# Performance work log

Measured on AMD Instinct MI355X. Metric: run time of the kernel, lower is better.

Reference implementation:

```python
import jax, jax.numpy as jnp
import numpy as np

D_MODEL = 1024
NUM_HEAD = 16
D_K = D_MODEL // NUM_HEAD


def setup_inputs() -> dict:
    key = jax.random.key(0)
    ks = jax.random.split(key, 9)
    s = 1.0 / np.sqrt(D_MODEL)
    x = jax.random.normal(ks[0], (2, 2048, D_MODEL), dtype=jnp.float32)
    Wq = jax.random.uniform(ks[1], (D_MODEL, D_MODEL), jnp.float32, -s, s)
    bq = jax.random.uniform(ks[2], (D_MODEL,), jnp.float32, -s, s)
    Wk = jax.random.uniform(ks[3], (D_MODEL, D_MODEL), jnp.float32, -s, s)
    bk = jax.random.uniform(ks[4], (D_MODEL,), jnp.float32, -s, s)
    Wv = jax.random.uniform(ks[5], (D_MODEL, D_MODEL), jnp.float32, -s, s)
    bv = jax.random.uniform(ks[6], (D_MODEL,), jnp.float32, -s, s)
    Wo = jax.random.uniform(ks[7], (D_MODEL, D_MODEL), jnp.float32, -s, s)
    bo = jax.random.uniform(ks[8], (D_MODEL,), jnp.float32, -s, s)
    return {"x": x, "Wq": Wq, "bq": bq, "Wk": Wk, "bk": bk,
            "Wv": Wv, "bv": bv, "Wo": Wo, "bo": bo}


def reference(x, Wq, bq, Wk, bk, Wv, bv, Wo, bo):
    b, n, d = x.shape
    h, dk = NUM_HEAD, D_K
    # Linear projections (torch Linear: x @ W.T + b)
    q = (x @ Wq.T + bq).reshape(b, n, h, dk).transpose(0, 2, 1, 3)  # [b,h,n,dk]
    k = (x @ Wk.T + bk).reshape(b, n, h, dk).transpose(0, 2, 1, 3)
    v = (x @ Wv.T + bv).reshape(b, n, h, dk).transpose(0, 2, 1, 3)
    scores = jnp.einsum('bhqd,bhkd->bhqk', q, k) / jnp.sqrt(jnp.float32(dk))
    attn = jax.nn.softmax(scores, axis=-1)  # [b,h,n,n]
    out = jnp.einsum('bhqk,bhkd->bhqd', attn, v)
    out = out.transpose(0, 2, 1, 3).reshape(b, n, d)
    return out @ Wo.T + bo
```

## Files before the change

### kernel.cpp

```cpp
#include <hip/hip_runtime.h>

#define BATCH   2
#define SEQ     2048
#define DMODEL  1024
#define NHEAD   16
#define DKH     64
#define MTOT    (BATCH*SEQ)
#define KDIM    DMODEL

#define XB    0u
#define WQB   (4u*1024u*1024u)
#define WKB   (5u*1024u*1024u)
#define WVB   (6u*1024u*1024u)
#define WOB   (7u*1024u*1024u)
#define QOFF  (8u*1024u*1024u)
#define KOFF  (12u*1024u*1024u)
#define VOFF  (16u*1024u*1024u)
#define OOFF  (20u*1024u*1024u)

typedef __bf16 bf16x8 __attribute__((ext_vector_type(8)));
typedef __bf16 bf16x4 __attribute__((ext_vector_type(4)));
typedef float  f32x4  __attribute__((ext_vector_type(4)));
typedef float  f32x16 __attribute__((ext_vector_type(16)));

__device__ __forceinline__ void async16(const __bf16* g, __bf16* l) {
  __builtin_amdgcn_global_load_lds(
      (const __attribute__((address_space(1))) void*)g,
      (__attribute__((address_space(3))) void*)l, 16, 0, 0);
}

__device__ __forceinline__ unsigned cvtpk_bf16(float lo, float hi) {
  unsigned r;
  asm("v_cvt_pk_bf16_f32 %0, %1, %2" : "=v"(r) : "v"(lo), "v"(hi));
  return r;
}
__device__ __forceinline__ void plswap(unsigned& a, unsigned& b) {
  asm("v_permlane32_swap_b32 %0, %1" : "+v"(a), "+v"(b));
}

__global__ __launch_bounds__(256) void cvt_fp32_bf16(
    const float* __restrict__ x,  const float* __restrict__ wq,
    const float* __restrict__ wk, const float* __restrict__ wv,
    const float* __restrict__ wo, __bf16* __restrict__ ws)
{
  const float* src; __bf16* dst; int n;
  switch (blockIdx.y) {
    case 0:  src = x;  dst = ws + XB;  n = 4 * 1024 * 1024; break;
    case 1:  src = wq; dst = ws + WQB; n = 1024 * 1024;     break;
    case 2:  src = wk; dst = ws + WKB; n = 1024 * 1024;     break;
    case 3:  src = wv; dst = ws + WVB; n = 1024 * 1024;     break;
    default: src = wo; dst = ws + WOB; n = 1024 * 1024;     break;
  }
  const int i = (blockIdx.x * 256 + threadIdx.x) * 8;
  if (i < n) {
    const float4 a = *(const float4*)(src + i);
    const float4 b = *(const float4*)(src + i + 4);
    bf16x8 o;
    o[0] = (__bf16)a.x; o[1] = (__bf16)a.y; o[2] = (__bf16)a.z; o[3] = (__bf16)a.w;
    o[4] = (__bf16)b.x; o[5] = (__bf16)b.y; o[6] = (__bf16)b.z; o[7] = (__bf16)b.w;
    *(bf16x8*)(dst + i) = o;
  }
}

__device__ __forceinline__ void gemm128_core(
    const __bf16* __restrict__ A, const __bf16* __restrict__ W,
    int m0, int n0, __bf16* lds, f32x4 (&acc)[4][4])
{
  __bf16* A_lds = lds;
  __bf16* B_lds = lds + 4096;
  const int t    = threadIdx.x;
  const int w    = t >> 6;
  const int lane = t & 63;
  const int ln15 = lane & 15;
  const int quad = lane >> 4;
  const int wr   = (w >> 1) << 6;
  const int wc   = (w & 1) << 6;

#pragma unroll
  for (int i = 0; i < 4; ++i)
#pragma unroll
    for (int j = 0; j < 4; ++j) acc[i][j] = (f32x4){0.f, 0.f, 0.f, 0.f};

  for (int kt = 0; kt < KDIM; kt += 32) {
    __syncthreads();
#pragma unroll
    for (int issue = 0; issue < 2; ++issue) {
      const int cbase = issue * 256 + (w << 6);
      const int c     = cbase + lane;
      const int row   = c >> 2;
      const int goff  = ((c & 3) ^ (row & 3)) << 3;
      async16(A + (size_t)(m0 + row) * KDIM + kt + goff, A_lds + cbase * 8);
      async16(W + (size_t)(n0 + row) * KDIM + kt + goff, B_lds + cbase * 8);
    }
    __syncthreads();

    bf16x8 af[4], bfr[4];
#pragma unroll
    for (int i = 0; i < 4; ++i) {
      const int row = wr + i * 16 + ln15;
      af[i] = *(const bf16x8*)&A_lds[row * 32 + ((quad ^ (row & 3)) << 3)];
    }
#pragma unroll
    for (int j = 0; j < 4; ++j) {
      const int row = wc + j * 16 + ln15;
      bfr[j] = *(const bf16x8*)&B_lds[row * 32 + ((quad ^ (row & 3)) << 3)];
    }
#pragma unroll
    for (int i = 0; i < 4; ++i)
#pragma unroll
      for (int j = 0; j < 4; ++j)
        acc[i][j] = __builtin_amdgcn_mfma_f32_16x16x32_bf16(af[i], bfr[j], acc[i][j], 0, 0, 0);
  }
}

__global__ __launch_bounds__(256) void qkv_gemm(
    const __bf16* __restrict__ X,
    const __bf16* __restrict__ Wq, const float* __restrict__ bq,
    const __bf16* __restrict__ Wk, const float* __restrict__ bk,
    const __bf16* __restrict__ Wv, const float* __restrict__ bv,
    __bf16* __restrict__ ws)
{
  __shared__ __align__(16) __bf16 lds[128 * 64];

  const int z = blockIdx.z;
  const __bf16* W    = (z == 0) ? Wq : (z == 1) ? Wk : Wv;
  const float*  bias = (z == 0) ? bq : (z == 1) ? bk : bv;
  __bf16* out = ws + ((z == 0) ? QOFF : (z == 1) ? KOFF : VOFF);
  const float scale = (z == 0) ? 0.125f * 1.44269504088896f : 1.0f;

  const int m0 = blockIdx.x * 128;
  const int n0 = blockIdx.y * 128;

  f32x4 acc[4][4];
  gemm128_core(X, W, m0, n0, lds, acc);

  const int t = threadIdx.x, w = t >> 6, lane = t & 63;
  const int ln15 = lane & 15, quad = lane >> 4;
  const int wr = (w >> 1) << 6, wc = (w & 1) << 6;

  float bj4[4];
#pragma unroll
  for (int j = 0; j < 4; ++j) bj4[j] = bias[n0 + wc + j * 16 + ln15];

  __syncthreads();
  __bf16* scr = lds + (w << 10);

  const int bb = m0 >> 11;
  const int s_base = (m0 & 2047) + wr;
  const int h = (n0 + wc) >> 6;

  if (z != 2) {
    const int rdrow = lane & 15, rdseg = lane >> 4;
#pragma unroll
    for (int i = 0; i < 4; ++i) {
#pragma unroll
      for (int j = 0; j < 4; ++j)
#pragma unroll
        for (int rr = 0; rr < 4; ++rr)
          scr[(quad * 4 + rr) * 64 + j * 16 + ln15] =
              (__bf16)((acc[i][j][rr] + bj4[j]) * scale);
      bf16x8 v0 = *(const bf16x8*)&scr[rdrow * 64 + rdseg * 16];
      bf16x8 v1 = *(const bf16x8*)&scr[rdrow * 64 + rdseg * 16 + 8];
      const int s = s_base + i * 16 + rdrow;
      __bf16* p = out + (((size_t)(bb * NHEAD + h)) * SEQ + s) * DKH + rdseg * 16;
      *(bf16x8*)p = v0;
      *(bf16x8*)&p[8] = v1;
    }
  } else {
#pragma unroll
    for (int i = 0; i < 4; ++i) {
#pragma unroll
      for (int j = 0; j < 4; ++j) {
        bf16x4 pk;
#pragma unroll
        for (int rr = 0; rr < 4; ++rr) pk[rr] = (__bf16)(acc[i][j][rr] + bj4[j]);
        *(bf16x4*)&scr[(j * 16 + ln15) * 16 + quad * 4] = pk;
      }
      bf16x8 c0 = *(const bf16x8*)&scr[lane * 16];
      bf16x8 c1 = *(const bf16x8*)&scr[lane * 16 + 8];
      __bf16* p = out + (((size_t)(bb * NHEAD + h)) * DKH + lane) * SEQ
                      + s_base + i * 16;
      *(bf16x8*)p = c0;
      *(bf16x8*)&p[8] = c1;
    }
  }
}

__global__ __launch_bounds__(256) void out_gemm(
    const __bf16* __restrict__ A, const __bf16* __restrict__ Wo,
    const float* __restrict__ bo, float* __restrict__ out)
{
  __shared__ __align__(16) __bf16 lds[6144];
  __bf16* A_lds = lds;
  __bf16* B_lds = lds + 2048;

  const int m0 = blockIdx.x * 64;
  const int n0 = blockIdx.y * 128;

  const int t = threadIdx.x, w = t >> 6, lane = t & 63;
  const int ln15 = lane & 15, quad = lane >> 4;

  f32x4 acc[4][2];
#pragma unroll
  for (int i = 0; i < 4; ++i)
#pragma unroll
    for (int j = 0; j < 2; ++j) acc[i][j] = (f32x4){0.f, 0.f, 0.f, 0.f};

  for (int kt = 0; kt < KDIM; kt += 32) {
    __syncthreads();
    {
      const int c = (w << 6) + lane;
      const int row = c >> 2;
      const int goff = ((c & 3) ^ (row & 3)) << 3;
      async16(A + (size_t)(m0 + row) * KDIM + kt + goff, A_lds + c * 8);
    }
#pragma unroll
    for (int issue = 0; issue < 2; ++issue) {
      const int cbase = issue * 256 + (w << 6);
      const int c = cbase + lane;
      const int row = c >> 2;
      const int goff = ((c & 3) ^ (row & 3)) << 3;
      async16(Wo + (size_t)(n0 + row) * KDIM + kt + goff, B_lds + cbase * 8);
    }
    __syncthreads();

    bf16x8 af[4], bfr[2];
#pragma unroll
    for (int i = 0; i < 4; ++i) {
      const int row = i * 16 + ln15;
      af[i] = *(const bf16x8*)&A_lds[row * 32 + ((quad ^ (row & 3)) << 3)];
    }
#pragma unroll
    for (int j = 0; j < 2; ++j) {
      const int row = (w << 5) + j * 16 + ln15;
      bfr[j] = *(const bf16x8*)&B_lds[row * 32 + ((quad ^ (row & 3)) << 3)];
    }
#pragma unroll
    for (int i = 0; i < 4; ++i)
#pragma unroll
      for (int j = 0; j < 2; ++j)
        acc[i][j] = __builtin_amdgcn_mfma_f32_16x16x32_bf16(af[i], bfr[j], acc[i][j], 0, 0, 0);
  }

  float bj2[2];
#pragma unroll
  for (int j = 0; j < 2; ++j) bj2[j] = bo[n0 + (w << 5) + j * 16 + ln15];

  __syncthreads();
  float* scrf = (float*)lds + (w << 9);

  const int rdrow = lane & 15, rdseg = lane >> 4;
#pragma unroll
  for (int i = 0; i < 4; ++i) {
#pragma unroll
    for (int j = 0; j < 2; ++j) {
      f32x4 v;
#pragma unroll
      for (int rr = 0; rr < 4; ++rr) v[rr] = acc[i][j][rr] + bj2[j];
      *(f32x4*)&scrf[(j * 16 + ln15) * 16 + quad * 4] = v;
    }
    const int m = m0 + i * 16 + rdrow;
    float* p = out + (size_t)m * DMODEL + n0 + (w << 5) + rdseg * 8;
#pragma unroll
    for (int cc = 0; cc < 2; ++cc) {
      f32x4 v;
#pragma unroll
      for (int e = 0; e < 4; ++e)
        v[e] = scrf[(rdseg * 8 + cc * 4 + e) * 16 + rdrow];
      *(f32x4*)&p[cc * 4] = v;
    }
  }
}

__device__ __forceinline__ void softmax_frag(const f32x16& s, float& l,
                                             bf16x8& pfa, bf16x8& pfb)
{
  float p[16];
#pragma unroll
  for (int r = 0; r < 16; ++r) {
    p[r] = __builtin_amdgcn_exp2f(s[r]);
    l += p[r];
  }
  unsigned A0 = cvtpk_bf16(p[0],  p[1]);
  unsigned A1 = cvtpk_bf16(p[2],  p[3]);
  unsigned B0 = cvtpk_bf16(p[4],  p[5]);
  unsigned B1 = cvtpk_bf16(p[6],  p[7]);
  unsigned C0 = cvtpk_bf16(p[8],  p[9]);
  unsigned C1 = cvtpk_bf16(p[10], p[11]);
  unsigned D0 = cvtpk_bf16(p[12], p[13]);
  unsigned D1 = cvtpk_bf16(p[14], p[15]);
  plswap(A0, B0);
  plswap(A1, B1);
  plswap(C0, D0);
  plswap(C1, D1);
  union { unsigned u[4]; bf16x8 v; } ua, ub;
  ua.u[0] = A0; ua.u[1] = A1; ua.u[2] = B0; ua.u[3] = B1;
  ub.u[0] = C0; ub.u[1] = C1; ub.u[2] = D0; ub.u[3] = D1;
  pfa = ua.v;
  pfb = ub.v;
}

__global__ __launch_bounds__(512, 4) void attn_kernel(
    const __bf16* __restrict__ Qb, const __bf16* __restrict__ Kb,
    const __bf16* __restrict__ Vtb, __bf16* __restrict__ Ob)
{
  __shared__ __align__(16) __bf16 smem[3 * 128 * 64];
  __bf16* QP = smem;
  __bf16* Ks = smem + 8192;
  __bf16* Vs = smem + 16384;

  const int t = threadIdx.x, w = t >> 6, lane = t & 63;
  const int ln31 = lane & 31, hl = lane >> 5;
  const int g  = w & 3;
  const int kh = w >> 2;
  const int bh = blockIdx.x;
  const int q0 = blockIdx.y * 128;
  const int bb = bh >> 4, hh = bh & 15;

  const __bf16* Qg = Qb + (size_t)bh * SEQ * DKH + (size_t)q0 * DKH;
  const __bf16* Kg = Kb + (size_t)bh * SEQ * DKH;
  const __bf16* Vg = Vtb + (size_t)bh * DKH * SEQ;

#pragma unroll
  for (int issue = 0; issue < 2; ++issue) {
    const int cbase = issue * 512 + (w << 6);
    const int c = cbase + lane;
    const int row = c >> 3;
    const int goff = ((c & 7) ^ (row & 7)) << 3;
    async16(Qg + (size_t)row * DKH + goff, QP + cbase * 8);
  }
  __syncthreads();

  const int qrow = (g << 5) + ln31;
  bf16x8 qf[4];
#pragma unroll
  for (int ks = 0; ks < 4; ++ks) {
    const int chunk = ((2 * ks + hl) ^ (qrow & 7));
    qf[ks] = *(const bf16x8*)&QP[qrow * 64 + (chunk << 3)];
  }

  float l_lane = 0.f;
  f32x16 o0, o1;
#pragma unroll
  for (int r = 0; r < 16; ++r) { o0[r] = 0.f; o1[r] = 0.f; }

#define PVSTEP(KS, PF) do {                                                   \
    const int vchunk = (kh << 3) + 2 * (KS) + hl;                             \
    bf16x8 vf0 = *(const bf16x8*)&Vs[ln31 * 128 +                             \
                                     ((vchunk ^ (ln31 & 15)) << 3)];          \
    bf16x8 vf1 = *(const bf16x8*)&Vs[(32 + ln31) * 128 +                      \
                                     ((vchunk ^ ((32 + ln31) & 15)) << 3)];   \
    o0 = __builtin_amdgcn_mfma_f32_32x32x16_bf16(PF, vf0, o0, 0, 0, 0);       \
    o1 = __builtin_amdgcn_mfma_f32_32x32x16_bf16(PF, vf1, o1, 0, 0, 0);       \
  } while (0)

  for (int kt = 0; kt < SEQ; kt += 128) {
    __syncthreads();
#pragma unroll
    for (int issue = 0; issue < 2; ++issue) {
      const int cbase = issue * 512 + (w << 6);
      const int c = cbase + lane;
      const int krow = c >> 3;
      const int kgoff = ((c & 7) ^ (krow & 7)) << 3;
      async16(Kg + (size_t)(kt + krow) * DKH + kgoff, Ks + cbase * 8);
      const int vrow = c >> 4;
      const int vgoff = ((c & 15) ^ (vrow & 15)) << 3;
      async16(Vg + (size_t)vrow * SEQ + kt + vgoff, Vs + cbase * 8);
    }
    __syncthreads();

    {
      f32x16 s;
#pragma unroll
      for (int r = 0; r < 16; ++r) s[r] = 0.f;
      const int kr = (kh << 6) + ln31;
      __builtin_amdgcn_s_setprio(1);
#pragma unroll
      for (int ks = 0; ks < 4; ++ks) {
        bf16x8 kf = *(const bf16x8*)&Ks[kr * 64 + (((2 * ks + hl) ^ (kr & 7)) << 3)];
        s = __builtin_amdgcn_mfma_f32_32x32x16_bf16(kf, qf[ks], s, 0, 0, 0);
      }
      __builtin_amdgcn_s_setprio(0);
      bf16x8 pa, pb;
      softmax_frag(s, l_lane, pa, pb);
      __builtin_amdgcn_s_setprio(1);
      PVSTEP(0, pa);
      PVSTEP(1, pb);
      __builtin_amdgcn_s_setprio(0);
    }
    {
      f32x16 s;
#pragma unroll
      for (int r = 0; r < 16; ++r) s[r] = 0.f;
      const int kr = (kh << 6) + 32 + ln31;
      __builtin_amdgcn_s_setprio(1);
#pragma unroll
      for (int ks = 0; ks < 4; ++ks) {
        bf16x8 kf = *(const bf16x8*)&Ks[kr * 64 + (((2 * ks + hl) ^ (kr & 7)) << 3)];
        s = __builtin_amdgcn_mfma_f32_32x32x16_bf16(kf, qf[ks], s, 0, 0, 0);
      }
      __builtin_amdgcn_s_setprio(0);
      bf16x8 pa, pb;
      softmax_frag(s, l_lane, pa, pb);
      __builtin_amdgcn_s_setprio(1);
      PVSTEP(2, pa);
      PVSTEP(3, pb);
      __builtin_amdgcn_s_setprio(0);
    }
  }
#undef PVSTEP

  __syncthreads();
  float* cmb = (float*)smem;
  const int dsw = ln31 & 7;
  l_lane += __shfl_xor(l_lane, 32);

  if (w >= 4) {
    float* base = cmb + (g << 11);
#pragma unroll
    for (int gg = 0; gg < 4; ++gg) {
      const int qq = ((2 * gg + hl) ^ dsw) << 2;
      f32x4 va, vb;
#pragma unroll
      for (int rr = 0; rr < 4; ++rr) { va[rr] = o0[4 * gg + rr]; vb[rr] = o1[4 * gg + rr]; }
      *(f32x4*)&base[ln31 * 32 + qq]        = va;
      *(f32x4*)&base[(32 + ln31) * 32 + qq] = vb;
    }
    if (hl == 0) cmb[8192 + (g << 5) + ln31] = l_lane;
  }
  __syncthreads();
  if (w < 4) {
    float* base = cmb + (g << 11);
#pragma unroll
    for (int gg = 0; gg < 4; ++gg) {
      const int qq = ((2 * gg + hl) ^ dsw) << 2;
      const f32x4 va = *(const f32x4*)&base[ln31 * 32 + qq];
      const f32x4 vb = *(const f32x4*)&base[(32 + ln31) * 32 + qq];
#pragma unroll
      for (int rr = 0; rr < 4; ++rr) { o0[4 * gg + rr] += va[rr]; o1[4 * gg + rr] += vb[rr]; }
    }
    const float inv = 1.0f / (l_lane + cmb[8192 + (g << 5) + ln31]);

#pragma unroll
    for (int r = 0; r < 16; ++r) {
      const int qi = (r & 3) + 8 * (r >> 2) + 4 * hl;
      const float iq = __shfl(inv, qi);
      const int q = q0 + (g << 5) + qi;
      __bf16* rowp = Ob + ((size_t)(bb * SEQ + q)) * DMODEL + hh * DKH;
      rowp[ln31]      = (__bf16)(o0[r] * iq);
      rowp[32 + ln31] = (__bf16)(o1[r] * iq);
    }
  }
}

extern "C" void kernel_launch(void* const* d_in, const int* in_sizes, int n_in,
                              void* d_out, int out_size, void* d_ws, size_t ws_size,
                              hipStream_t stream)
{
  const float* x  = (const float*)d_in[0];
  const float* Wq = (const float*)d_in[1];
  const float* bq = (const float*)d_in[2];
  const float* Wk = (const float*)d_in[3];
  const float* bk = (const float*)d_in[4];
  const float* Wv = (const float*)d_in[5];
  const float* bv = (const float*)d_in[6];
  const float* Wo = (const float*)d_in[7];
  const float* bo = (const float*)d_in[8];
  float*  out = (float*)d_out;
  __bf16* ws  = (__bf16*)d_ws;

  cvt_fp32_bf16<<<dim3(2048, 5, 1), 256, 0, stream>>>(x, Wq, Wk, Wv, Wo, ws);

  qkv_gemm<<<dim3(MTOT / 128, DMODEL / 128, 3), 256, 0, stream>>>(
      ws + XB, ws + WQB, bq, ws + WKB, bk, ws + WVB, bv, ws);

  attn_kernel<<<dim3(BATCH * NHEAD, SEQ / 128), 512, 0, stream>>>(
      ws + QOFF, ws + KOFF, ws + VOFF, ws + OOFF);

  out_gemm<<<dim3(MTOT / 64, DMODEL / 128), 256, 0, stream>>>(
      ws + OOFF, ws + WOB, bo, out);
}
```

Before: 186.7 us.

## Double-buffer LDS tiles in QKV, output GEMM and attention kernels

Converts the K-loops of the QKV projection GEMM, the output GEMM and the attention kernel to a two-stage ping-pong LDS scheme. The next tile's async global-to-LDS copy is issued before computing on the current tile, removing one barrier per step and overlapping memory latency with MFMA work. In exchange, LDS per block roughly doubles. For attention it grows from 48KB to 80KB, which may cut how many 512-thread blocks fit per CU.

```diff
diff --git a/kernel.cpp b/kernel.cpp
--- a/kernel.cpp
+++ b/kernel.cpp
@@ -62,12 +62,47 @@
   }
 }
 
+__device__ __forceinline__ void gemm_stage128(
+    const __bf16* __restrict__ A, const __bf16* __restrict__ W,
+    int m0, int n0, int kt, __bf16* A_l, __bf16* B_l, int w, int lane)
+{
+#pragma unroll
+  for (int issue = 0; issue < 2; ++issue) {
+    const int cbase = issue * 256 + (w << 6);
+    const int c     = cbase + lane;
+    const int row   = c >> 2;
+    const int goff  = ((c & 3) ^ (row & 3)) << 3;
+    async16(A + (size_t)(m0 + row) * KDIM + kt + goff, A_l + cbase * 8);
+    async16(W + (size_t)(n0 + row) * KDIM + kt + goff, B_l + cbase * 8);
+  }
+}
+
+__device__ __forceinline__ void gemm_step128(
+    const __bf16* A_lds, const __bf16* B_lds,
+    int wr, int wc, int ln15, int quad, f32x4 (&acc)[4][4])
+{
+  bf16x8 af[4], bfr[4];
+#pragma unroll
+  for (int i = 0; i < 4; ++i) {
+    const int row = wr + i * 16 + ln15;
+    af[i] = *(const bf16x8*)&A_lds[row * 32 + ((quad ^ (row & 3)) << 3)];
+  }
+#pragma unroll
+  for (int j = 0; j < 4; ++j) {
+    const int row = wc + j * 16 + ln15;
+    bfr[j] = *(const bf16x8*)&B_lds[row * 32 + ((quad ^ (row & 3)) << 3)];
+  }
+#pragma unroll
+  for (int i = 0; i < 4; ++i)
+#pragma unroll
+    for (int j = 0; j < 4; ++j)
+      acc[i][j] = __builtin_amdgcn_mfma_f32_16x16x32_bf16(af[i], bfr[j], acc[i][j], 0, 0, 0);
+}
+
 __device__ __forceinline__ void gemm128_core(
     const __bf16* __restrict__ A, const __bf16* __restrict__ W,
     int m0, int n0, __bf16* lds, f32x4 (&acc)[4][4])
 {
-  __bf16* A_lds = lds;
-  __bf16* B_lds = lds + 4096;
   const int t    = threadIdx.x;
   const int w    = t >> 6;
   const int lane = t & 63;
@@ -81,35 +116,17 @@
 #pragma unroll
     for (int j = 0; j < 4; ++j) acc[i][j] = (f32x4){0.f, 0.f, 0.f, 0.f};
 
-  for (int kt = 0; kt < KDIM; kt += 32) {
+  gemm_stage128(A, W, m0, n0, 0, lds, lds + 4096, w, lane);
+  __syncthreads();
+
+  for (int kt = 0; kt < KDIM; kt += 64) {
+    gemm_stage128(A, W, m0, n0, kt + 32, lds + 8192, lds + 12288, w, lane);
+    gemm_step128(lds, lds + 4096, wr, wc, ln15, quad, acc);
     __syncthreads();
-#pragma unroll
-    for (int issue = 0; issue < 2; ++issue) {
-      const int cbase = issue * 256 + (w << 6);
-      const int c     = cbase + lane;
-      const int row   = c >> 2;
-      const int goff  = ((c & 3) ^ (row & 3)) << 3;
-      async16(A + (size_t)(m0 + row) * KDIM + kt + goff, A_lds + cbase * 8);
-      async16(W + (size_t)(n0 + row) * KDIM + kt + goff, B_lds + cbase * 8);
-    }
+    if (kt + 64 < KDIM)
+      gemm_stage128(A, W, m0, n0, kt + 64, lds, lds + 4096, w, lane);
+    gemm_step128(lds + 8192, lds + 12288, wr, wc, ln15, quad, acc);
     __syncthreads();
-
-    bf16x8 af[4], bfr[4];
-#pragma unroll
-    for (int i = 0; i < 4; ++i) {
-      const int row = wr + i * 16 + ln15;
-      af[i] = *(const bf16x8*)&A_lds[row * 32 + ((quad ^ (row & 3)) << 3)];
-    }
-#pragma unroll
-    for (int j = 0; j < 4; ++j) {
-      const int row = wc + j * 16 + ln15;
-      bfr[j] = *(const bf16x8*)&B_lds[row * 32 + ((quad ^ (row & 3)) << 3)];
-    }
-#pragma unroll
-    for (int i = 0; i < 4; ++i)
-#pragma unroll
-      for (int j = 0; j < 4; ++j)
-        acc[i][j] = __builtin_amdgcn_mfma_f32_16x16x32_bf16(af[i], bfr[j], acc[i][j], 0, 0, 0);
   }
 }
 
@@ -120,7 +137,7 @@
     const __bf16* __restrict__ Wv, const float* __restrict__ bv,
     __bf16* __restrict__ ws)
 {
-  __shared__ __align__(16) __bf16 lds[128 * 64];
+  __shared__ __align__(16) __bf16 lds[16384];
 
   const int z = blockIdx.z;
   const __bf16* W    = (z == 0) ? Wq : (z == 1) ? Wk : Wv;
@@ -186,13 +203,57 @@
   }
 }
 
+__device__ __forceinline__ void out_stage(
+    const __bf16* __restrict__ A, const __bf16* __restrict__ Wo,
+    int m0, int n0, int kt, __bf16* A_l, __bf16* B_l, int w, int lane)
+{
+  {
+    const int c = (w << 6) + lane;
+    const int row = c >> 2;
+    const int goff = ((c & 3) ^ (row & 3)) << 3;
+    async16(A + (size_t)(m0 + row) * KDIM + kt + goff, A_l + c * 8);
+  }
+#pragma unroll
+  for (int issue = 0; issue < 2; ++issue) {
+    const int cbase = issue * 256 + (w << 6);
+    const int c = cbase + lane;
+    const int row = c >> 2;
+    const int goff = ((c & 3) ^ (row & 3)) << 3;
+    async16(Wo + (size_t)(n0 + row) * KDIM + kt + goff, B_l + cbase * 8);
+  }
+}
+
+__device__ __forceinline__ void out_step(
+    const __bf16* A_lds, const __bf16* B_lds,
+    int w, int ln15, int quad, f32x4 (&acc)[4][2])
+{
+  bf16x8 af[4], bfr[2];
+#pragma unroll
+  for (int i = 0; i < 4; ++i) {
+    const int row = i * 16 + ln15;
+    af[i] = *(const bf16x8*)&A_lds[row * 32 + ((quad ^ (row & 3)) << 3)];
+  }
+#pragma unroll
+  for (int j = 0; j < 2; ++j) {
+    const int row = (w << 5) + j * 16 + ln15;
+    bfr[j] = *(const bf16x8*)&B_lds[row * 32 + ((quad ^ (row & 3)) << 3)];
+  }
+#pragma unroll
+  for (int i = 0; i < 4; ++i)
+#pragma unroll
+    for (int j = 0; j < 2; ++j)
+      acc[i][j] = __builtin_amdgcn_mfma_f32_16x16x32_bf16(af[i], bfr[j], acc[i][j], 0, 0, 0);
+}
+
 __global__ __launch_bounds__(256) void out_gemm(
     const __bf16* __restrict__ A, const __bf16* __restrict__ Wo,
     const float* __restrict__ bo, float* __restrict__ out)
 {
-  __shared__ __align__(16) __bf16 lds[6144];
-  __bf16* A_lds = lds;
-  __bf16* B_lds = lds + 2048;
+  __shared__ __align__(16) __bf16 lds[12288];
+  __bf16* A0 = lds;
+  __bf16* B0 = lds + 2048;
+  __bf16* A1 = lds + 6144;
+  __bf16* B1 = lds + 8192;
 
   const int m0 = blockIdx.x * 64;
   const int n0 = blockIdx.y * 128;
@@ -206,47 +267,23 @@
 #pragma unroll
     for (int j = 0; j < 2; ++j) acc[i][j] = (f32x4){0.f, 0.f, 0.f, 0.f};
 
-  for (int kt = 0; kt < KDIM; kt += 32) {
+  out_stage(A, Wo, m0, n0, 0, A0, B0, w, lane);
+  __syncthreads();
+
+  for (int kt = 0; kt < KDIM; kt += 64) {
+    out_stage(A, Wo, m0, n0, kt + 32, A1, B1, w, lane);
+    out_step(A0, B0, w, ln15, quad, acc);
     __syncthreads();
-    {
-      const int c = (w << 6) + lane;
-      const int row = c >> 2;
-      const int goff = ((c & 3) ^ (row & 3)) << 3;
-      async16(A + (size_t)(m0 + row) * KDIM + kt + goff, A_lds + c * 8);
-    }
-#pragma unroll
-    for (int issue = 0; issue < 2; ++issue) {
-      const int cbase = issue * 256 + (w << 6);
-      const int c = cbase + lane;
-      const int row = c >> 2;
-      const int goff = ((c & 3) ^ (row & 3)) << 3;
-      async16(Wo + (size_t)(n0 + row) * KDIM + kt + goff, B_lds + cbase * 8);
-    }
+    if (kt + 64 < KDIM)
+      out_stage(A, Wo, m0, n0, kt + 64, A0, B0, w, lane);
+    out_step(A1, B1, w, ln15, quad, acc);
     __syncthreads();
-
-    bf16x8 af[4], bfr[2];
-#pragma unroll
-    for (int i = 0; i < 4; ++i) {
-      const int row = i * 16 + ln15;
-      af[i] = *(const bf16x8*)&A_lds[row * 32 + ((quad ^ (row & 3)) << 3)];
-    }
-#pragma unroll
-    for (int j = 0; j < 2; ++j) {
-      const int row = (w << 5) + j * 16 + ln15;
-      bfr[j] = *(const bf16x8*)&B_lds[row * 32 + ((quad ^ (row & 3)) << 3)];
-    }
-#pragma unroll
-    for (int i = 0; i < 4; ++i)
-#pragma unroll
-      for (int j = 0; j < 2; ++j)
-        acc[i][j] = __builtin_amdgcn_mfma_f32_16x16x32_bf16(af[i], bfr[j], acc[i][j], 0, 0, 0);
   }
 
   float bj2[2];
 #pragma unroll
   for (int j = 0; j < 2; ++j) bj2[j] = bo[n0 + (w << 5) + j * 16 + ln15];
 
-  __syncthreads();
   float* scrf = (float*)lds + (w << 9);
 
   const int rdrow = lane & 15, rdseg = lane >> 4;
@@ -300,14 +337,54 @@
   pfb = ub.v;
 }
 
+__device__ __forceinline__ void pvstep(const __bf16* Vs, int kh, int KS, int hl,
+                                       int ln31, const bf16x8& PF,
+                                       f32x16& o0, f32x16& o1)
+{
+  const int vchunk = (kh << 3) + 2 * KS + hl;
+  bf16x8 vf0 = *(const bf16x8*)&Vs[ln31 * 128 + ((vchunk ^ (ln31 & 15)) << 3)];
+  bf16x8 vf1 = *(const bf16x8*)&Vs[(32 + ln31) * 128 +
+                                   ((vchunk ^ ((32 + ln31) & 15)) << 3)];
+  o0 = __builtin_amdgcn_mfma_f32_32x32x16_bf16(PF, vf0, o0, 0, 0, 0);
+  o1 = __builtin_amdgcn_mfma_f32_32x32x16_bf16(PF, vf1, o1, 0, 0, 0);
+}
+
+__device__ __forceinline__ void attn_tile_compute(
+    const __bf16* Ks, const __bf16* Vs, const bf16x8 (&qf)[4],
+    int kh, int ln31, int hl, float& l_lane, f32x16& o0, f32x16& o1)
+{
+#pragma unroll
+  for (int half = 0; half < 2; ++half) {
+    f32x16 s;
+#pragma unroll
+    for (int r = 0; r < 16; ++r) s[r] = 0.f;
+    const int kr = (kh << 6) + half * 32 + ln31;
+    __builtin_amdgcn_s_setprio(1);
+#pragma unroll
+    for (int ks = 0; ks < 4; ++ks) {
+      bf16x8 kf = *(const bf16x8*)&Ks[kr * 64 + (((2 * ks + hl) ^ (kr & 7)) << 3)];
+      s = __builtin_amdgcn_mfma_f32_32x32x16_bf16(kf, qf[ks], s, 0, 0, 0);
+    }
+    __builtin_amdgcn_s_setprio(0);
+    bf16x8 pa, pb;
+    softmax_frag(s, l_lane, pa, pb);
+    __builtin_amdgcn_s_setprio(1);
+    pvstep(Vs, kh, half * 2 + 0, hl, ln31, pa, o0, o1);
+    pvstep(Vs, kh, half * 2 + 1, hl, ln31, pb, o0, o1);
+    __builtin_amdgcn_s_setprio(0);
+  }
+}
+
 __global__ __launch_bounds__(512, 4) void attn_kernel(
     const __bf16* __restrict__ Qb, const __bf16* __restrict__ Kb,
     const __bf16* __restrict__ Vtb, __bf16* __restrict__ Ob)
 {
-  __shared__ __align__(16) __bf16 smem[3 * 128 * 64];
+  __shared__ __align__(16) __bf16 smem[5 * 128 * 64];
   __bf16* QP = smem;
-  __bf16* Ks = smem + 8192;
-  __bf16* Vs = smem + 16384;
+  __bf16* K0 = smem + 8192;
+  __bf16* V0 = smem + 16384;
+  __bf16* K1 = smem + 24576;
+  __bf16* V1 = smem + 32768;
 
   const int t = threadIdx.x, w = t >> 6, lane = t & 63;
   const int ln31 = lane & 31, hl = lane >> 5;
@@ -321,41 +398,7 @@
   const __bf16* Kg = Kb + (size_t)bh * SEQ * DKH;
   const __bf16* Vg = Vtb + (size_t)bh * DKH * SEQ;
 
-#pragma unroll
-  for (int issue = 0; issue < 2; ++issue) {
-    const int cbase = issue * 512 + (w << 6);
-    const int c = cbase + lane;
-    const int row = c >> 3;
-    const int goff = ((c & 7) ^ (row & 7)) << 3;
-    async16(Qg + (size_t)row * DKH + goff, QP + cbase * 8);
-  }
-  __syncthreads();
-
-  const int qrow = (g << 5) + ln31;
-  bf16x8 qf[4];
-#pragma unroll
-  for (int ks = 0; ks < 4; ++ks) {
-    const int chunk = ((2 * ks + hl) ^ (qrow & 7));
-    qf[ks] = *(const bf16x8*)&QP[qrow * 64 + (chunk << 3)];
-  }
-
-  float l_lane = 0.f;
-  f32x16 o0, o1;
-#pragma unroll
-  for (int r = 0; r < 16; ++r) { o0[r] = 0.f; o1[r] = 0.f; }
-
-#define PVSTEP(KS, PF) do {                                                   \
-    const int vchunk = (kh << 3) + 2 * (KS) + hl;                             \
-    bf16x8 vf0 = *(const bf16x8*)&Vs[ln31 * 128 +                             \
-                                     ((vchunk ^ (ln31 & 15)) << 3)];          \
-    bf16x8 vf1 = *(const bf16x8*)&Vs[(32 + ln31) * 128 +                      \
-                                     ((vchunk ^ ((32 + ln31) & 15)) << 3)];   \
-    o0 = __builtin_amdgcn_mfma_f32_32x32x16_bf16(PF, vf0, o0, 0, 0, 0);       \
-    o1 = __builtin_amdgcn_mfma_f32_32x32x16_bf16(PF, vf1, o1, 0, 0, 0);       \
-  } while (0)
-
-  for (int kt = 0; kt < SEQ; kt += 128) {
-    __syncthreads();
+  auto stage_kv = [&](int kt, __bf16* Ks, __bf16* Vs) {
 #pragma unroll
     for (int issue = 0; issue < 2; ++issue) {
       const int cbase = issue * 512 + (w << 6);
@@ -367,50 +410,42 @@
       const int vgoff = ((c & 15) ^ (vrow & 15)) << 3;
       async16(Vg + (size_t)vrow * SEQ + kt + vgoff, Vs + cbase * 8);
     }
+  };
+
+#pragma unroll
+  for (int issue = 0; issue < 2; ++issue) {
+    const int cbase = issue * 512 + (w << 6);
+    const int c = cbase + lane;
+    const int row = c >> 3;
+    const int goff = ((c & 7) ^ (row & 7)) << 3;
+    async16(Qg + (size_t)row * DKH + goff, QP + cbase * 8);
+  }
+  stage_kv(0, K0, V0);
+  __syncthreads();
+
+  const int qrow = (g << 5) + ln31;
+  bf16x8 qf[4];
+#pragma unroll
+  for (int ks = 0; ks < 4; ++ks) {
+    const int chunk = ((2 * ks + hl) ^ (qrow & 7));
+    qf[ks] = *(const bf16x8*)&QP[qrow * 64 + (chunk << 3)];
+  }
+
+  float l_lane = 0.f;
+  f32x16 o0, o1;
+#pragma unroll
+  for (int r = 0; r < 16; ++r) { o0[r] = 0.f; o1[r] = 0.f; }
+
+  for (int kt = 0; kt < SEQ; kt += 256) {
+    stage_kv(kt + 128, K1, V1);
+    attn_tile_compute(K0, V0, qf, kh, ln31, hl, l_lane, o0, o1);
     __syncthreads();
-
-    {
-      f32x16 s;
-#pragma unroll
-      for (int r = 0; r < 16; ++r) s[r] = 0.f;
-      const int kr = (kh << 6) + ln31;
-      __builtin_amdgcn_s_setprio(1);
-#pragma unroll
-      for (int ks = 0; ks < 4; ++ks) {
-        bf16x8 kf = *(const bf16x8*)&Ks[kr * 64 + (((2 * ks + hl) ^ (kr & 7)) << 3)];
-        s = __builtin_amdgcn_mfma_f32_32x32x16_bf16(kf, qf[ks], s, 0, 0, 0);
-      }
-      __builtin_amdgcn_s_setprio(0);
-      bf16x8 pa, pb;
-      softmax_frag(s, l_lane, pa, pb);
-      __builtin_amdgcn_s_setprio(1);
-      PVSTEP(0, pa);
-      PVSTEP(1, pb);
-      __builtin_amdgcn_s_setprio(0);
-    }
-    {
-      f32x16 s;
-#pragma unroll
-      for (int r = 0; r < 16; ++r) s[r] = 0.f;
-      const int kr = (kh << 6) + 32 + ln31;
-      __builtin_amdgcn_s_setprio(1);
-#pragma unroll
-      for (int ks = 0; ks < 4; ++ks) {
-        bf16x8 kf = *(const bf16x8*)&Ks[kr * 64 + (((2 * ks + hl) ^ (kr & 7)) << 3)];
-        s = __builtin_amdgcn_mfma_f32_32x32x16_bf16(kf, qf[ks], s, 0, 0, 0);
-      }
-      __builtin_amdgcn_s_setprio(0);
-      bf16x8 pa, pb;
-      softmax_frag(s, l_lane, pa, pb);
-      __builtin_amdgcn_s_setprio(1);
-      PVSTEP(2, pa);
-      PVSTEP(3, pb);
-      __builtin_amdgcn_s_setprio(0);
-    }
-  }
-#undef PVSTEP
-
-  __syncthreads();
+    if (kt + 256 < SEQ)
+      stage_kv(kt + 256, K0, V0);
+    attn_tile_compute(K1, V1, qf, kh, ln31, hl, l_lane, o0, o1);
+    __syncthreads();
+  }
+
   float* cmb = (float*)smem;
   const int dsw = ln31 & 7;
   l_lane += __shfl_xor(l_lane, 32);
```

New measurement: 192.7 us. 1.03x slower.
